# Kernel tuning notes

Hardware: AMD Instinct MI355X
Metric: run time of the kernel (lower is better)

Reference implementation:

```python
import jax, jax.numpy as jnp
import numpy as np

B, T, D = 64, 2048, 512

def setup_inputs() -> dict:
    key = jax.random.key(0)
    k1, k2, k3, k4, k5 = jax.random.split(key, 5)
    s = 1.0 / np.sqrt(2 * D)  # torch Linear default init scale
    return {
        "sequence": jax.random.normal(k1, (B, T, D), dtype=jnp.float32),
        "W_gate": jax.random.uniform(k2, (2 * D, D), jnp.float32, -s, s),
        "b_gate": jax.random.uniform(k3, (D,), jnp.float32, -s, s),
        "W_cand": jax.random.uniform(k4, (2 * D, D), jnp.float32, -s, s),
        "b_cand": jax.random.uniform(k5, (D,), jnp.float32, -s, s),
    }

def _recurrence(sequence, W_gate, b_gate, W_cand, b_cand):
    # sequence: [B, T, D]; hidden: [B, D]
    h0 = jnp.zeros((sequence.shape[0], sequence.shape[-1]), sequence.dtype)

    def step(hidden, x_t):
        joined = jnp.concatenate([hidden, x_t], axis=-1)  # [B, 2D]
        gate = jax.nn.sigmoid(joined @ W_gate + b_gate)
        cand = jnp.tanh(joined @ W_cand + b_cand)
        hidden = gate * hidden + (1.0 - gate) * cand
        return hidden, None

    # scan over time: move T to leading axis
    h_final, _ = jax.lax.scan(step, h0, jnp.swapaxes(sequence, 0, 1))
    return h_final

def reference(sequence, W_gate, b_gate, W_cand, b_cand):
    return _recurrence(sequence, W_gate, b_gate, W_cand, b_cand)
```

## Files before the change

kernel.cpp:

```cpp
#include <hip/hip_runtime.h>

typedef unsigned short u16;
typedef unsigned int u32;
typedef unsigned long long u64;
typedef __attribute__((ext_vector_type(8))) short bf16x8;
typedef __attribute__((ext_vector_type(4))) float f32x4;

#define TT 2048
#define BB 64
#define DDIM 512

__device__ __forceinline__ float bf2f(u16 u) {
  union { u32 i; float f; } c; c.i = ((u32)u) << 16; return c.f;
}
__device__ __forceinline__ u16 f2bf(float f) {
  union { float f; u32 i; } c; c.f = f;
  u32 r = c.i + 0x7fffu + ((c.i >> 16) & 1u);
  return (u16)(r >> 16);
}

__global__ void cvt_seq(const float* __restrict__ x, u16* __restrict__ xb, long n4) {
  long i = (long)blockIdx.x * blockDim.x + threadIdx.x;
  long stride = (long)gridDim.x * blockDim.x;
  for (long idx = i; idx < n4; idx += stride) {
    float4 v = ((const float4*)x)[idx];
    ushort4 o;
    o.x = f2bf(v.x); o.y = f2bf(v.y); o.z = f2bf(v.z); o.w = f2bf(v.w);
    ((ushort4*)xb)[idx] = o;
  }
}

__global__ void prep_w(const float* __restrict__ Wg, const float* __restrict__ Wc,
                       const float* __restrict__ bg, const float* __restrict__ bc,
                       u16* __restrict__ Wht, u16* __restrict__ Wxt, float* __restrict__ bias) {
  int n = blockIdx.x;
  const float* src = (n < 512) ? Wg : Wc;
  int d = n & 511;
  for (int k = threadIdx.x; k < 512; k += blockDim.x) {
    Wht[(long)n * 512 + k] = f2bf(src[(long)k * 512 + d]);
    Wxt[(long)n * 512 + k] = f2bf(src[(long)(512 + k) * 512 + d]);
  }
  if (threadIdx.x == 0) bias[n] = (n < 512) ? bg[d] : bc[d];
}

__global__ __launch_bounds__(256, 2) void gemm_x(
    const u16* __restrict__ Xb, const u16* __restrict__ Wxt,
    const float* __restrict__ bias, u16* __restrict__ C) {
  __shared__ u16 lA[2][128 * 64];
  __shared__ u16 lB[2][128 * 64];
  const int tid = threadIdx.x;
  const int w = tid >> 6, l = tid & 63;
  const int lrow = l & 15, lk = l >> 4;
  int bid = blockIdx.x;
  int xcd = bid & 7, q = bid >> 3;
  long m0 = ((long)xcd * 128 + (q >> 3)) * 128;
  int n0 = (q & 7) * 128;

  f32x4 acc[4][4];
#pragma unroll
  for (int i = 0; i < 4; ++i)
#pragma unroll
    for (int j = 0; j < 4; ++j) acc[i][j] = (f32x4){0.f, 0.f, 0.f, 0.f};

  auto stage = [&](int p, int kt) {
#pragma unroll
    for (int ii = 0; ii < 4; ++ii) {
      int c = w * 4 + ii;
      int row = c * 8 + (l >> 3);
      int kb = ((l & 7) * 16) ^ ((row & 7) << 4);
      int koff = kt * 64 + (kb >> 1);
      __builtin_amdgcn_global_load_lds(
          (__attribute__((address_space(1))) unsigned*)(Wxt + (long)(n0 + row) * 512 + koff),
          (__attribute__((address_space(3))) unsigned*)(&lA[p][c * 512]), 16, 0, 0);
      __builtin_amdgcn_global_load_lds(
          (__attribute__((address_space(1))) unsigned*)(Xb + (m0 + row) * 512 + koff),
          (__attribute__((address_space(3))) unsigned*)(&lB[p][c * 512]), 16, 0, 0);
    }
  };
  auto compute = [&](int p) {
#pragma unroll
    for (int ks = 0; ks < 2; ++ks) {
      bf16x8 af[4], bv[4];
#pragma unroll
      for (int i = 0; i < 4; ++i) {
        int rowa = (w & 1) * 64 + i * 16 + lrow;
        int kba = (ks * 64 + lk * 16) ^ ((rowa & 7) << 4);
        af[i] = *(const bf16x8*)((const char*)lA[p] + rowa * 128 + kba);
        int rowb = (w >> 1) * 64 + i * 16 + lrow;
        int kbb = (ks * 64 + lk * 16) ^ ((rowb & 7) << 4);
        bv[i] = *(const bf16x8*)((const char*)lB[p] + rowb * 128 + kbb);
      }
#pragma unroll
      for (int i = 0; i < 4; ++i)
#pragma unroll
        for (int j = 0; j < 4; ++j)
          acc[i][j] = __builtin_amdgcn_mfma_f32_16x16x32_bf16(af[i], bv[j], acc[i][j], 0, 0, 0);
    }
  };

  stage(0, 0);
  asm volatile("s_waitcnt vmcnt(0)" ::: "memory");
  __syncthreads();
  for (int kt = 0; kt < 8; ++kt) {
    int p = kt & 1;
    if (kt < 7) stage(p ^ 1, kt + 1);
    compute(p);
    asm volatile("s_waitcnt vmcnt(0)" ::: "memory");
    __syncthreads();
  }
#pragma unroll
  for (int i = 0; i < 4; ++i) {
    int n = n0 + (w & 1) * 64 + i * 16 + lk * 4;
    float4 bvv = *(const float4*)&bias[n];
#pragma unroll
    for (int j = 0; j < 4; ++j) {
      long crow = m0 + (w >> 1) * 64 + j * 16 + lrow;
      ushort4 o;
      o.x = f2bf(acc[i][j][0] + bvv.x);
      o.y = f2bf(acc[i][j][1] + bvv.y);
      o.z = f2bf(acc[i][j][2] + bvv.z);
      o.w = f2bf(acc[i][j][3] + bvv.w);
      *(ushort4*)(C + crow * 1024 + n) = o;
    }
  }
}

__global__ __launch_bounds__(256, 1) void recur(
    const u16* __restrict__ Wht, const u16* __restrict__ GxCx,
    u16* __restrict__ hbuf, float* __restrict__ out, u32* __restrict__ flags) {
  const int tid = threadIdx.x;
  const int w = tid >> 6, l = tid & 63;
  const int lrow = l & 15, lk = l >> 4;
  const int wg = blockIdx.x;
  const int g = wg >> 3, s = wg & 7;

  const int b = g * 16 + lrow;
  const int drow = s * 64 + w * 16 + lrow;
  const int d0 = s * 64 + w * 16 + lk * 4;

  bf16x8 wgf[16], wcf[16];
#pragma unroll
  for (int ks = 0; ks < 16; ++ks) {
    wgf[ks] = *(const bf16x8*)(Wht + (long)drow * 512 + ks * 32 + lk * 8);
    wcf[ks] = *(const bf16x8*)(Wht + (long)(512 + drow) * 512 + ks * 32 + lk * 8);
  }

  u32* myflag = &flags[(wg * 4 + w) * 16];
  const u32* fp = &flags[(g * 32 + (l & 31)) * 16];
  float hold[4] = {0.f, 0.f, 0.f, 0.f};

#pragma unroll 1
  for (int t = 0; t < TT; ++t) {
    long m = (long)b * TT + t;
    ushort4 gx4 = *(const ushort4*)(GxCx + m * 1024 + d0);
    ushort4 cx4 = *(const ushort4*)(GxCx + m * 1024 + 512 + d0);

    f32x4 ag0 = {0, 0, 0, 0}, ag1 = {0, 0, 0, 0}, ac0 = {0, 0, 0, 0}, ac1 = {0, 0, 0, 0};
    if (t > 0) {
      u32 it = 0;
      while (__hip_atomic_load(fp, __ATOMIC_RELAXED, __HIP_MEMORY_SCOPE_AGENT) < (u32)t) {
        if (++it > 50000u) break;
      }

      const u16* hb = hbuf + ((long)(t & 1) * 64 + g * 16) * 512;
      bf16x8 hfr[16];
#pragma unroll
      for (int ks = 0; ks < 16; ++ks) {
        const u16* p = hb + lrow * 512 + ks * 32 + lk * 8;
        union { u64 q[2]; bf16x8 v; } u;
        u.q[0] = __hip_atomic_load((const u64*)p, __ATOMIC_RELAXED, __HIP_MEMORY_SCOPE_AGENT);
        u.q[1] = __hip_atomic_load((const u64*)(p + 4), __ATOMIC_RELAXED, __HIP_MEMORY_SCOPE_AGENT);
        hfr[ks] = u.v;
      }
#pragma unroll
      for (int ks = 0; ks < 16; ks += 2) {
        ag0 = __builtin_amdgcn_mfma_f32_16x16x32_bf16(wgf[ks], hfr[ks], ag0, 0, 0, 0);
        ac0 = __builtin_amdgcn_mfma_f32_16x16x32_bf16(wcf[ks], hfr[ks], ac0, 0, 0, 0);
        ag1 = __builtin_amdgcn_mfma_f32_16x16x32_bf16(wgf[ks + 1], hfr[ks + 1], ag1, 0, 0, 0);
        ac1 = __builtin_amdgcn_mfma_f32_16x16x32_bf16(wcf[ks + 1], hfr[ks + 1], ac1, 0, 0, 0);
      }
    }

    float pg[4] = {ag0[0] + ag1[0] + bf2f(gx4.x), ag0[1] + ag1[1] + bf2f(gx4.y),
                   ag0[2] + ag1[2] + bf2f(gx4.z), ag0[3] + ag1[3] + bf2f(gx4.w)};
    float pc[4] = {ac0[0] + ac1[0] + bf2f(cx4.x), ac0[1] + ac1[1] + bf2f(cx4.y),
                   ac0[2] + ac1[2] + bf2f(cx4.z), ac0[3] + ac1[3] + bf2f(cx4.w)};
    float hn[4];
#pragma unroll
    for (int r = 0; r < 4; ++r) {
      float gt = 1.f / (1.f + __expf(-pg[r]));
      float cd = 1.f - 2.f / (1.f + __expf(2.f * pc[r]));
      hn[r] = gt * hold[r] + (1.f - gt) * cd;
      hold[r] = hn[r];
    }

    if (t == TT - 1) {
      float4 o = {hn[0], hn[1], hn[2], hn[3]};
      *(float4*)(out + (long)b * 512 + d0) = o;
    } else {
      ushort4 hv;
      hv.x = f2bf(hn[0]); hv.y = f2bf(hn[1]); hv.z = f2bf(hn[2]); hv.w = f2bf(hn[3]);
      union { ushort4 s4; u64 q; } pu; pu.s4 = hv;
      u16* dst = hbuf + ((long)((t + 1) & 1) * 64 + b) * 512 + d0;
      __hip_atomic_store((u64*)dst, pu.q, __ATOMIC_RELAXED, __HIP_MEMORY_SCOPE_AGENT);
      asm volatile("s_waitcnt vmcnt(0)" ::: "memory");
      if (l == 0)
        __hip_atomic_fetch_add(myflag, 1u, __ATOMIC_RELAXED, __HIP_MEMORY_SCOPE_AGENT);
    }
  }
}

extern "C" void kernel_launch(void* const* d_in, const int* in_sizes, int n_in,
                              void* d_out, int out_size, void* d_ws, size_t ws_size,
                              hipStream_t stream) {
  const float* seq = (const float*)d_in[0];
  const float* Wg = (const float*)d_in[1];
  const float* bg = (const float*)d_in[2];
  const float* Wc = (const float*)d_in[3];
  const float* bc = (const float*)d_in[4];
  float* out = (float*)d_out;

  const size_t XB_BYTES = (size_t)BB * TT * DDIM * 2;
  const size_t GXCX_BYTES = (size_t)BB * TT * 2 * DDIM * 2;
  const size_t WHT_BYTES = 1024 * 512 * 2;
  const size_t WXT_BYTES = 1024 * 512 * 2;
  const size_t BIAS_BYTES = 1024 * 4;
  const size_t HBUF_BYTES = 2 * 64 * 512 * 2;
  const size_t FLAG_BYTES = 128 * 16 * 4;

  char* ws = (char*)d_ws;
  u16* Xb = (u16*)ws;
  u16* GxCx = (u16*)(ws + XB_BYTES);
  u16* Wht = (u16*)(ws + XB_BYTES + GXCX_BYTES);
  u16* Wxt = (u16*)(ws + XB_BYTES + GXCX_BYTES + WHT_BYTES);
  float* biasb = (float*)(ws + XB_BYTES + GXCX_BYTES + WHT_BYTES + WXT_BYTES);
  u16* hbuf = (u16*)(ws + XB_BYTES + GXCX_BYTES + WHT_BYTES + WXT_BYTES + BIAS_BYTES);
  u32* flags = (u32*)(ws + XB_BYTES + GXCX_BYTES + WHT_BYTES + WXT_BYTES + BIAS_BYTES + HBUF_BYTES);
  (void)ws_size; (void)in_sizes; (void)n_in; (void)out_size;

  hipMemsetAsync(flags, 0, FLAG_BYTES, stream);

  cvt_seq<<<2048, 256, 0, stream>>>(seq, Xb, (long)BB * TT * DDIM / 4);
  prep_w<<<1024, 256, 0, stream>>>(Wg, Wc, bg, bc, Wht, Wxt, biasb);
  gemm_x<<<8192, 256, 0, stream>>>(Xb, Wxt, biasb, GxCx);
  recur<<<32, 256, 0, stream>>>(Wht, GxCx, hbuf, out, flags);
}
```

Measured before the change: 12.75 ms.

## Replace flag-based step sync with tagged hidden-state words polled directly

Drops the separate per-wave flag counters and the store-then-wait-then-flag sequence. Each hidden-state pair is now written as a 64-bit word holding a step tag in the upper half, and consumers poll the data itself until every tag matches the current step. This takes a full memory round trip and the vmcnt drain off the critical path of every step, at the cost of doubling the hidden-state traffic and re-reading the whole fragment on each polling round. It also depends on the workspace not holding stale matching tags, since the flag memset was removed.

```diff
diff --git a/kernel.cpp b/kernel.cpp
--- a/kernel.cpp
+++ b/kernel.cpp
@@ -127,7 +127,7 @@
 
 __global__ __launch_bounds__(256, 1) void recur(
     const u16* __restrict__ Wht, const u16* __restrict__ GxCx,
-    u16* __restrict__ hbuf, float* __restrict__ out, u32* __restrict__ flags) {
+    u64* __restrict__ hb64, float* __restrict__ out) {
   const int tid = threadIdx.x;
   const int w = tid >> 6, l = tid & 63;
   const int lrow = l & 15, lk = l >> 4;
@@ -145,8 +145,9 @@
     wcf[ks] = *(const bf16x8*)(Wht + (long)(512 + drow) * 512 + ks * 32 + lk * 8);
   }
 
-  u32* myflag = &flags[(wg * 4 + w) * 16];
-  const u32* fp = &flags[(g * 32 + (l & 31)) * 16];
+  const u64* grow = hb64 + (long)b * 256;
+  u64* prow = hb64 + (long)b * 256 + (d0 >> 1);
+
   float hold[4] = {0.f, 0.f, 0.f, 0.f};
 
 #pragma unroll 1
@@ -157,27 +158,34 @@
 
     f32x4 ag0 = {0, 0, 0, 0}, ag1 = {0, 0, 0, 0}, ac0 = {0, 0, 0, 0}, ac1 = {0, 0, 0, 0};
     if (t > 0) {
-      u32 it = 0;
-      while (__hip_atomic_load(fp, __ATOMIC_RELAXED, __HIP_MEMORY_SCOPE_AGENT) < (u32)t) {
-        if (++it > 50000u) break;
+      const u64* src = grow + (long)(t & 1) * (64 * 256);
+      const u32 tagv = (u32)t;
+      u64 q[64];
+      for (int round = 0; round < 16384; ++round) {
+        u32 bad = 0;
+#pragma unroll
+        for (int ks = 0; ks < 16; ++ks) {
+#pragma unroll
+          for (int j = 0; j < 4; ++j) {
+            q[ks * 4 + j] = __hip_atomic_load(src + ks * 16 + lk * 4 + j,
+                                              __ATOMIC_RELAXED, __HIP_MEMORY_SCOPE_AGENT);
+            bad |= ((u32)(q[ks * 4 + j] >> 32)) ^ tagv;
+          }
+        }
+        if (__all(bad == 0)) break;
       }
-
-      const u16* hb = hbuf + ((long)(t & 1) * 64 + g * 16) * 512;
-      bf16x8 hfr[16];
-#pragma unroll
-      for (int ks = 0; ks < 16; ++ks) {
-        const u16* p = hb + lrow * 512 + ks * 32 + lk * 8;
-        union { u64 q[2]; bf16x8 v; } u;
-        u.q[0] = __hip_atomic_load((const u64*)p, __ATOMIC_RELAXED, __HIP_MEMORY_SCOPE_AGENT);
-        u.q[1] = __hip_atomic_load((const u64*)(p + 4), __ATOMIC_RELAXED, __HIP_MEMORY_SCOPE_AGENT);
-        hfr[ks] = u.v;
-      }
 #pragma unroll
       for (int ks = 0; ks < 16; ks += 2) {
-        ag0 = __builtin_amdgcn_mfma_f32_16x16x32_bf16(wgf[ks], hfr[ks], ag0, 0, 0, 0);
-        ac0 = __builtin_amdgcn_mfma_f32_16x16x32_bf16(wcf[ks], hfr[ks], ac0, 0, 0, 0);
-        ag1 = __builtin_amdgcn_mfma_f32_16x16x32_bf16(wgf[ks + 1], hfr[ks + 1], ag1, 0, 0, 0);
-        ac1 = __builtin_amdgcn_mfma_f32_16x16x32_bf16(wcf[ks + 1], hfr[ks + 1], ac1, 0, 0, 0);
+        union { u32 w4[4]; bf16x8 v; } ua, ub;
+#pragma unroll
+        for (int j = 0; j < 4; ++j) {
+          ua.w4[j] = (u32)q[ks * 4 + j];
+          ub.w4[j] = (u32)q[ks * 4 + 4 + j];
+        }
+        ag0 = __builtin_amdgcn_mfma_f32_16x16x32_bf16(wgf[ks], ua.v, ag0, 0, 0, 0);
+        ac0 = __builtin_amdgcn_mfma_f32_16x16x32_bf16(wcf[ks], ua.v, ac0, 0, 0, 0);
+        ag1 = __builtin_amdgcn_mfma_f32_16x16x32_bf16(wgf[ks + 1], ub.v, ag1, 0, 0, 0);
+        ac1 = __builtin_amdgcn_mfma_f32_16x16x32_bf16(wcf[ks + 1], ub.v, ac1, 0, 0, 0);
       }
     }
 
@@ -198,14 +206,12 @@
       float4 o = {hn[0], hn[1], hn[2], hn[3]};
       *(float4*)(out + (long)b * 512 + d0) = o;
     } else {
-      ushort4 hv;
-      hv.x = f2bf(hn[0]); hv.y = f2bf(hn[1]); hv.z = f2bf(hn[2]); hv.w = f2bf(hn[3]);
-      union { ushort4 s4; u64 q; } pu; pu.s4 = hv;
-      u16* dst = hbuf + ((long)((t + 1) & 1) * 64 + b) * 512 + d0;
-      __hip_atomic_store((u64*)dst, pu.q, __ATOMIC_RELAXED, __HIP_MEMORY_SCOPE_AGENT);
-      asm volatile("s_waitcnt vmcnt(0)" ::: "memory");
-      if (l == 0)
-        __hip_atomic_fetch_add(myflag, 1u, __ATOMIC_RELAXED, __HIP_MEMORY_SCOPE_AGENT);
+      const u64 tg = (u64)(u32)(t + 1) << 32;
+      u64 s0 = tg | (u32)((u32)f2bf(hn[1]) << 16 | f2bf(hn[0]));
+      u64 s1 = tg | (u32)((u32)f2bf(hn[3]) << 16 | f2bf(hn[2]));
+      u64* dst = prow + (long)((t + 1) & 1) * (64 * 256);
+      __hip_atomic_store(dst, s0, __ATOMIC_RELAXED, __HIP_MEMORY_SCOPE_AGENT);
+      __hip_atomic_store(dst + 1, s1, __ATOMIC_RELAXED, __HIP_MEMORY_SCOPE_AGENT);
     }
   }
 }
@@ -225,8 +231,6 @@
   const size_t WHT_BYTES = 1024 * 512 * 2;
   const size_t WXT_BYTES = 1024 * 512 * 2;
   const size_t BIAS_BYTES = 1024 * 4;
-  const size_t HBUF_BYTES = 2 * 64 * 512 * 2;
-  const size_t FLAG_BYTES = 128 * 16 * 4;
 
   char* ws = (char*)d_ws;
   u16* Xb = (u16*)ws;
@@ -234,14 +238,11 @@
   u16* Wht = (u16*)(ws + XB_BYTES + GXCX_BYTES);
   u16* Wxt = (u16*)(ws + XB_BYTES + GXCX_BYTES + WHT_BYTES);
   float* biasb = (float*)(ws + XB_BYTES + GXCX_BYTES + WHT_BYTES + WXT_BYTES);
-  u16* hbuf = (u16*)(ws + XB_BYTES + GXCX_BYTES + WHT_BYTES + WXT_BYTES + BIAS_BYTES);
-  u32* flags = (u32*)(ws + XB_BYTES + GXCX_BYTES + WHT_BYTES + WXT_BYTES + BIAS_BYTES + HBUF_BYTES);
+  u64* hb64 = (u64*)(ws + XB_BYTES + GXCX_BYTES + WHT_BYTES + WXT_BYTES + BIAS_BYTES);
   (void)ws_size; (void)in_sizes; (void)n_in; (void)out_size;
-
-  hipMemsetAsync(flags, 0, FLAG_BYTES, stream);
 
   cvt_seq<<<2048, 256, 0, stream>>>(seq, Xb, (long)BB * TT * DDIM / 4);
   prep_w<<<1024, 256, 0, stream>>>(Wg, Wc, bg, bc, Wht, Wxt, biasb);
   gemm_x<<<8192, 256, 0, stream>>>(Xb, Wxt, biasb, GxCx);
-  recur<<<32, 256, 0, stream>>>(Wht, GxCx, hbuf, out, flags);
-}
+  recur<<<32, 256, 0, stream>>>(Wht, GxCx, hb64, out);
+}
```

Measured after the change: 29.00 ms. 128% more time.
